# Kernel optimization log

Hardware: AMD Instinct MI355X
Metric: run time of the kernel (lower is better)

The kernel has to match this reference:

```python
import jax, jax.numpy as jnp
import numpy as np

B, C, F, H, W = 8, 16, 256, 112, 112   # batch, cells/image, channels, height, width
NB = 3                                  # tgt_shape = (3, 3) adaptive pool bins


def setup_inputs() -> dict:
    key = jax.random.key(0)
    kf, ky, kx, kry, krx, kn = jax.random.split(key, 6)
    feature_maps = jax.random.normal(kf, (B, F, H, W), jnp.float32)
    N = B * C
    # random rectangular cell blobs with bernoulli interior holes + guaranteed core
    cy = jax.random.randint(ky, (N, 1, 1), 20, H - 20)
    cx = jax.random.randint(kx, (N, 1, 1), 20, W - 20)
    ry = jax.random.randint(kry, (N, 1, 1), 5, 18)
    rx = jax.random.randint(krx, (N, 1, 1), 5, 18)
    yy = jnp.arange(H)[None, :, None]
    xx = jnp.arange(W)[None, None, :]
    rect = (jnp.abs(yy - cy) <= ry) & (jnp.abs(xx - cx) <= rx)
    noise = jax.random.bernoulli(kn, 0.8, (N, H, W))
    core = (jnp.abs(yy - cy) <= 2) & (jnp.abs(xx - cx) <= 2)
    cell_masks = rect & (noise | core)            # [N, H, W] bool, each nonempty
    cell_counts = jnp.full((B,), C, jnp.int32)    # fixed cells per image
    return {"feature_maps": feature_maps, "cell_masks": cell_masks,
            "cell_counts": cell_counts}


def _bin_membership(lo, hi, length):
    # adaptive-pool bin i covers [lo + floor(i*sz/NB), lo + ceil((i+1)*sz/NB))
    i = jnp.arange(NB)
    sz = (hi - lo)[..., None]                      # [B, C, 1]
    start = lo[..., None] + (i * sz) // NB         # [B, C, NB]
    end = lo[..., None] + ((i + 1) * sz + NB - 1) // NB
    pos = jnp.arange(length)
    return (pos >= start[..., None]) & (pos < end[..., None])  # [B, C, NB, L]


def reference(feature_maps, cell_masks, cell_counts):
    Bv, Fv, Hv, Wv = feature_maps.shape
    Cv = cell_masks.shape[0] // Bv
    masks = cell_masks.reshape(Bv, Cv, Hv, Wv)
    # tight bbox per cell (first/last True row and column, exclusive end)
    rows = masks.any(-1)                            # [B, C, H]
    cols = masks.any(-2)                            # [B, C, W]
    y0 = jnp.argmax(rows, -1)
    y1 = Hv - jnp.argmax(rows[..., ::-1], -1)
    x0 = jnp.argmax(cols, -1)
    x1 = Wv - jnp.argmax(cols[..., ::-1], -1)
    ymem = _bin_membership(y0, y1, Hv)              # [B, C, NB, H]
    xmem = _bin_membership(x0, x1, Wv)              # [B, C, NB, W]
    neg = jnp.finfo(feature_maps.dtype).min
    feat = feature_maps[:, None]                    # [B, 1, F, H, W]
    m = masks[:, :, None]                           # [B, C, 1, H, W]
    pooled = []
    for i in range(NB):
        ym = ymem[:, :, i][:, :, None, :, None]     # [B, C, 1, H, 1]
        for j in range(NB):
            xm = xmem[:, :, j][:, :, None, None, :]  # [B, C, 1, 1, W]
            inbin = ym & xm
            # inside bin & mask -> feature; inside bin & ~mask -> 0 (zeroed crop);
            # outside bin -> -inf (excluded from max)
            v = jnp.where(inbin & m, feat, jnp.where(inbin, 0.0, neg))
            pooled.append(v.max((-1, -2)))          # [B, C, F]
    out = jnp.stack(pooled, -1)                     # [B, C, F, 9], index = i*NB + j
    # matches torch pooled.view(-1): flatten order f*9 + i*3 + j
    return out.reshape(Bv * Cv, Fv * NB * NB)
```

## Files before the change

### kernel.cpp

```cpp
#include <hip/hip_runtime.h>
#include <float.h>

#define B_  8
#define C_  16
#define N_  (B_*C_)
#define F_  256
#define H_  112
#define W_  112
#define HW_ (H_*W_)
#define NB_ 3
#define FPW 4
#define WPB 4
#define FPB (FPW*WPB)


__global__ __launch_bounds__(256) void bbox_kernel(const int* __restrict__ mask,
                                                   int* __restrict__ bb) {
    int n = blockIdx.x;
    int t = threadIdx.x;
    __shared__ int rowsAny[H_];
    __shared__ int colsAny[W_];
    __shared__ int smin[256];
    __shared__ int smax[256];
    if (t < H_) rowsAny[t] = 0;
    if (t < W_) colsAny[t] = 0;
    __syncthreads();
    const int* m = mask + (size_t)n * HW_;
    for (int idx = t; idx < HW_; idx += 256) {
        if (m[idx]) {
            int y = idx / W_;
            int x = idx - y * W_;
            rowsAny[y] = 1;
            colsAny[x] = 1;
        }
    }
    __syncthreads();
    smin[t] = (t < H_ && rowsAny[t]) ? t : 0x3fffffff;
    smax[t] = (t < H_ && rowsAny[t]) ? t : -1;
    __syncthreads();
    #pragma unroll
    for (int s = 128; s > 0; s >>= 1) {
        if (t < s) { smin[t] = min(smin[t], smin[t+s]); smax[t] = max(smax[t], smax[t+s]); }
        __syncthreads();
    }
    int y0 = smin[0], y1 = smax[0] + 1;
    __syncthreads();
    smin[t] = (t < W_ && colsAny[t]) ? t : 0x3fffffff;
    smax[t] = (t < W_ && colsAny[t]) ? t : -1;
    __syncthreads();
    #pragma unroll
    for (int s = 128; s > 0; s >>= 1) {
        if (t < s) { smin[t] = min(smin[t], smin[t+s]); smax[t] = max(smax[t], smax[t+s]); }
        __syncthreads();
    }
    if (t == 0) {
        int x0 = smin[0], x1 = smax[0] + 1;
        int* o = bb + n * 16;
        o[0] = y0; o[1] = y1; o[2] = x0; o[3] = x1;
        int szy = y1 - y0, szx = x1 - x0;
        for (int i = 0; i < NB_; ++i) {
            o[4+i]  = y0 + (i*szy)/NB_;
            o[7+i]  = y0 + ((i+1)*szy + NB_-1)/NB_;
            o[10+i] = x0 + (i*szx)/NB_;
            o[13+i] = x0 + ((i+1)*szx + NB_-1)/NB_;
        }
    }
}

__global__ __launch_bounds__(256) void pool_kernel(
        const float* __restrict__ feat, const int* __restrict__ mask,
        const int* __restrict__ bb, float* __restrict__ out) {
    int n = blockIdx.x;
    int b = n >> 4;
    const int* o = bb + n * 16;
    int y0 = o[0], x0 = o[2];
    int bh = o[1] - y0, bw = o[3] - x0;

    __shared__ float lmask[37 * 37];
    {
        const int* mbase = mask + (size_t)n * HW_ + (size_t)y0 * W_ + x0;
        int tot = bh * bw;
        for (int idx = threadIdx.x; idx < tot; idx += 256) {
            int dy = idx / bw, dx = idx - dy * bw;
            lmask[idx] = mbase[dy * W_ + dx] ? 1.0f : 0.0f;
        }
    }
    __syncthreads();

    int wave = threadIdx.x >> 6, lane = threadIdx.x & 63;
    int laneC = lane < bw ? lane : bw - 1;
    int f0 = blockIdx.y * FPB + wave * FPW;
    const float* p = feat + (size_t)(b * F_ + f0) * HW_ + (size_t)y0 * W_ + x0 + laneC;

    int ys0 = o[4], ys1 = o[5], ys2 = o[6];
    int ye0 = o[7], ye1 = o[8], ye2 = o[9];

    float acc[3][FPW];
    #pragma unroll
    for (int i = 0; i < 3; ++i)
        #pragma unroll
        for (int k = 0; k < FPW; ++k) acc[i][k] = -FLT_MAX;

    float fv[FPW];
    #pragma unroll
    for (int k = 0; k < FPW; ++k) fv[k] = p[k * HW_];

    for (int dy = 0; dy < bh; ++dy) {
        int dyn = (dy + 1 < bh) ? dy + 1 : dy;
        int offn = dyn * W_;
        float nv[FPW];
        #pragma unroll
        for (int k = 0; k < FPW; ++k) nv[k] = p[k * HW_ + offn];

        float mv = lmask[dy * bw + laneC];
        int y = y0 + dy;
        bool in0 = (y >= ys0) & (y < ye0);
        bool in1 = (y >= ys1) & (y < ye1);
        bool in2 = (y >= ys2) & (y < ye2);
        #pragma unroll
        for (int k = 0; k < FPW; ++k) {
            float v = mv * fv[k];
            if (in0) acc[0][k] = fmaxf(acc[0][k], v);
            if (in1) acc[1][k] = fmaxf(acc[1][k], v);
            if (in2) acc[2][k] = fmaxf(acc[2][k], v);
        }
        #pragma unroll
        for (int k = 0; k < FPW; ++k) fv[k] = nv[k];
    }

    int x = x0 + lane;
    int xs[3] = {o[10], o[11], o[12]};
    int xe[3] = {o[13], o[14], o[15]};

    #pragma unroll
    for (int k = 0; k < FPW; ++k) {
        float st = 0.0f;
        #pragma unroll
        for (int i = 0; i < 3; ++i) {
            #pragma unroll
            for (int j = 0; j < 3; ++j) {
                float val = (x >= xs[j] && x < xe[j]) ? acc[i][k] : -FLT_MAX;
                #pragma unroll
                for (int off = 32; off; off >>= 1)
                    val = fmaxf(val, __shfl_xor(val, off));
                st = (lane == i * 3 + j) ? val : st;
            }
        }
        if (lane < 9) out[(size_t)(n * F_ + f0 + k) * 9 + lane] = st;
    }
}

extern "C" void kernel_launch(void* const* d_in, const int* in_sizes, int n_in,
                              void* d_out, int out_size, void* d_ws, size_t ws_size,
                              hipStream_t stream) {
    const float* feat = (const float*)d_in[0];
    const int*   mask = (const int*)d_in[1];
    int* bb = (int*)d_ws;

    bbox_kernel<<<N_, 256, 0, stream>>>(mask, bb);
    dim3 grid(N_, F_ / FPB);
    pool_kernel<<<grid, 256, 0, stream>>>(feat, mask, bb, (float*)d_out);
}
```

Measured before the change: 197.4 us.

## Vectorize bbox scan with int4 loads and pool with float4 row tiles

The bbox kernel now reads the mask as int4, keeps per-thread min/max of rows and columns, and reduces them with wave shuffles instead of shared flag arrays and tree reductions. The pool kernel remaps each wave so 16 lanes cover 64 aligned columns with float4 loads and 4 lane groups cover 4 rows per step. It processes 2 channels in parallel over 2 sequential passes, with the shared mask padded to 64 columns. The aim is to cut the number of load instructions and the serial per-row loop, at the cost of more accumulator registers and 9 shuffle reductions per channel.

```diff
diff --git a/kernel.cpp b/kernel.cpp
--- a/kernel.cpp
+++ b/kernel.cpp
@@ -9,52 +9,50 @@
 #define W_  112
 #define HW_ (H_*W_)
 #define NB_ 3
-#define FPW 4
-#define WPB 4
-#define FPB (FPW*WPB)
+
+#define FPAR 2
+#define FSEQ 2
+#define FPW  (FPAR*FSEQ)
+#define WPB  4
+#define FPB  (FPW*WPB)
+#define LMS  64
 
 
-__global__ __launch_bounds__(256) void bbox_kernel(const int* __restrict__ mask,
+__global__ __launch_bounds__(256) void bbox_kernel(const int4* __restrict__ mask4,
                                                    int* __restrict__ bb) {
-    int n = blockIdx.x;
-    int t = threadIdx.x;
-    __shared__ int rowsAny[H_];
-    __shared__ int colsAny[W_];
-    __shared__ int smin[256];
-    __shared__ int smax[256];
-    if (t < H_) rowsAny[t] = 0;
-    if (t < W_) colsAny[t] = 0;
-    __syncthreads();
-    const int* m = mask + (size_t)n * HW_;
-    for (int idx = t; idx < HW_; idx += 256) {
-        if (m[idx]) {
-            int y = idx / W_;
-            int x = idx - y * W_;
-            rowsAny[y] = 1;
-            colsAny[x] = 1;
-        }
+    int n = blockIdx.x, t = threadIdx.x;
+    const int4* m = mask4 + (size_t)n * (HW_ / 4);
+    int ymin = 1 << 20, ymax = -1, xmin = 1 << 20, xmax = -1;
+    for (int i = t; i < HW_ / 4; i += 256) {
+        int4 v = m[i];
+        int y = i / 28;
+        int xb = (i - y * 28) * 4;
+        if (v.x | v.y | v.z | v.w) { ymin = min(ymin, y); ymax = max(ymax, y); }
+        if (v.x) { xmin = min(xmin, xb);     xmax = max(xmax, xb);     }
+        if (v.y) { xmin = min(xmin, xb + 1); xmax = max(xmax, xb + 1); }
+        if (v.z) { xmin = min(xmin, xb + 2); xmax = max(xmax, xb + 2); }
+        if (v.w) { xmin = min(xmin, xb + 3); xmax = max(xmax, xb + 3); }
+    }
+    #pragma unroll
+    for (int off = 32; off; off >>= 1) {
+        ymin = min(ymin, __shfl_xor(ymin, off));
+        ymax = max(ymax, __shfl_xor(ymax, off));
+        xmin = min(xmin, __shfl_xor(xmin, off));
+        xmax = max(xmax, __shfl_xor(xmax, off));
+    }
+    __shared__ int red[4][4];
+    int wave = t >> 6;
+    if ((t & 63) == 0) {
+        red[wave][0] = ymin; red[wave][1] = ymax;
+        red[wave][2] = xmin; red[wave][3] = xmax;
     }
     __syncthreads();
-    smin[t] = (t < H_ && rowsAny[t]) ? t : 0x3fffffff;
-    smax[t] = (t < H_ && rowsAny[t]) ? t : -1;
-    __syncthreads();
-    #pragma unroll
-    for (int s = 128; s > 0; s >>= 1) {
-        if (t < s) { smin[t] = min(smin[t], smin[t+s]); smax[t] = max(smax[t], smax[t+s]); }
-        __syncthreads();
-    }
-    int y0 = smin[0], y1 = smax[0] + 1;
-    __syncthreads();
-    smin[t] = (t < W_ && colsAny[t]) ? t : 0x3fffffff;
-    smax[t] = (t < W_ && colsAny[t]) ? t : -1;
-    __syncthreads();
-    #pragma unroll
-    for (int s = 128; s > 0; s >>= 1) {
-        if (t < s) { smin[t] = min(smin[t], smin[t+s]); smax[t] = max(smax[t], smax[t+s]); }
-        __syncthreads();
-    }
     if (t == 0) {
-        int x0 = smin[0], x1 = smax[0] + 1;
+        for (int w = 1; w < 4; ++w) {
+            ymin = min(ymin, red[w][0]); ymax = max(ymax, red[w][1]);
+            xmin = min(xmin, red[w][2]); xmax = max(xmax, red[w][3]);
+        }
+        int y0 = ymin, y1 = ymax + 1, x0 = xmin, x1 = xmax + 1;
         int* o = bb + n * 16;
         o[0] = y0; o[1] = y1; o[2] = x0; o[3] = x1;
         int szy = y1 - y0, szx = x1 - x0;
@@ -75,78 +73,111 @@
     const int* o = bb + n * 16;
     int y0 = o[0], x0 = o[2];
     int bh = o[1] - y0, bw = o[3] - x0;
+    int x0a = x0 & ~3;
+    int woff = x0 - x0a;
+    int x1 = x0 + bw;
 
-    __shared__ float lmask[37 * 37];
-    {
-        const int* mbase = mask + (size_t)n * HW_ + (size_t)y0 * W_ + x0;
-        int tot = bh * bw;
-        for (int idx = threadIdx.x; idx < tot; idx += 256) {
-            int dy = idx / bw, dx = idx - dy * bw;
-            lmask[idx] = mbase[dy * W_ + dx] ? 1.0f : 0.0f;
-        }
+    __shared__ float lm[37 * LMS];
+    for (int idx = threadIdx.x; idx < bh * LMS; idx += 256) {
+        int dy = idx >> 6, xo = idx & 63;
+        int gx = x0a + xo;
+        float v = 0.0f;
+        if (gx >= x0 && gx < x1)
+            v = mask[(size_t)n * HW_ + (size_t)(y0 + dy) * W_ + gx] ? 1.0f : 0.0f;
+        lm[idx] = v;
     }
     __syncthreads();
 
-    int wave = threadIdx.x >> 6, lane = threadIdx.x & 63;
-    int laneC = lane < bw ? lane : bw - 1;
+    int lane = threadIdx.x & 63, wave = threadIdx.x >> 6;
+    int xq = lane & 15, rg = lane >> 4;
+    int xq4  = (4 * xq < woff + bw) ? 4 * xq : 0;
     int f0 = blockIdx.y * FPB + wave * FPW;
-    const float* p = feat + (size_t)(b * F_ + f0) * HW_ + (size_t)y0 * W_ + x0 + laneC;
 
     int ys0 = o[4], ys1 = o[5], ys2 = o[6];
     int ye0 = o[7], ye1 = o[8], ye2 = o[9];
+    int xs0 = o[10], xs1 = o[11], xs2 = o[12];
+    int xe0 = o[13], xe1 = o[14], xe2 = o[15];
 
-    float acc[3][FPW];
-    #pragma unroll
-    for (int i = 0; i < 3; ++i)
+    int ntiles = (bh + 3) >> 2;
+    int bhm1 = bh - 1;
+    const float* gbase = feat + (size_t)(b * F_) * HW_ + (size_t)y0 * W_ + x0a + xq4;
+
+    for (int fs = 0; fs < FSEQ; ++fs) {
+        int f = f0 + fs * FPAR;
+        const float* gp0 = gbase + (size_t)f * HW_;
+        const float* gp1 = gp0 + HW_;
+
+        float acc[3][4][FPAR];
         #pragma unroll
-        for (int k = 0; k < FPW; ++k) acc[i][k] = -FLT_MAX;
+        for (int i = 0; i < 3; ++i)
+            #pragma unroll
+            for (int s = 0; s < 4; ++s)
+                #pragma unroll
+                for (int pp = 0; pp < FPAR; ++pp) acc[i][s][pp] = -FLT_MAX;
 
-    float fv[FPW];
-    #pragma unroll
-    for (int k = 0; k < FPW; ++k) fv[k] = p[k * HW_];
+        int dy0 = min(rg, bhm1);
+        float4 cur0 = *(const float4*)(gp0 + dy0 * W_);
+        float4 cur1 = *(const float4*)(gp1 + dy0 * W_);
 
-    for (int dy = 0; dy < bh; ++dy) {
-        int dyn = (dy + 1 < bh) ? dy + 1 : dy;
-        int offn = dyn * W_;
-        float nv[FPW];
+        for (int t = 0; t < ntiles; ++t) {
+            int tn = (t + 1 < ntiles) ? t + 1 : t;
+            int dyn = min(4 * tn + rg, bhm1);
+            float4 nxt0 = *(const float4*)(gp0 + dyn * W_);
+            float4 nxt1 = *(const float4*)(gp1 + dyn * W_);
+
+            int dyc = min(4 * t + rg, bhm1);
+            float4 mv = *(const float4*)(&lm[dyc * LMS + 4 * xq]);
+            int y = y0 + dyc;
+            bool in0 = (y >= ys0) & (y < ye0);
+            bool in1 = (y >= ys1) & (y < ye1);
+            bool in2 = (y >= ys2) & (y < ye2);
+
+            float v0[4] = {mv.x * cur0.x, mv.y * cur0.y, mv.z * cur0.z, mv.w * cur0.w};
+            float v1[4] = {mv.x * cur1.x, mv.y * cur1.y, mv.z * cur1.z, mv.w * cur1.w};
+            #pragma unroll
+            for (int s = 0; s < 4; ++s) {
+                if (in0) { acc[0][s][0] = fmaxf(acc[0][s][0], v0[s]);
+                           acc[0][s][1] = fmaxf(acc[0][s][1], v1[s]); }
+                if (in1) { acc[1][s][0] = fmaxf(acc[1][s][0], v0[s]);
+                           acc[1][s][1] = fmaxf(acc[1][s][1], v1[s]); }
+                if (in2) { acc[2][s][0] = fmaxf(acc[2][s][0], v0[s]);
+                           acc[2][s][1] = fmaxf(acc[2][s][1], v1[s]); }
+            }
+            cur0 = nxt0; cur1 = nxt1;
+        }
+
+        int xg = x0a + 4 * xq;
         #pragma unroll
-        for (int k = 0; k < FPW; ++k) nv[k] = p[k * HW_ + offn];
-
-        float mv = lmask[dy * bw + laneC];
-        int y = y0 + dy;
-        bool in0 = (y >= ys0) & (y < ye0);
-        bool in1 = (y >= ys1) & (y < ye1);
-        bool in2 = (y >= ys2) & (y < ye2);
-        #pragma unroll
-        for (int k = 0; k < FPW; ++k) {
-            float v = mv * fv[k];
-            if (in0) acc[0][k] = fmaxf(acc[0][k], v);
-            if (in1) acc[1][k] = fmaxf(acc[1][k], v);
-            if (in2) acc[2][k] = fmaxf(acc[2][k], v);
+        for (int pp = 0; pp < FPAR; ++pp) {
+            float part[9];
+            #pragma unroll
+            for (int i = 0; i < 3; ++i) {
+                #pragma unroll
+                for (int s = 0; s < 4; ++s) {
+                    int xx = xg + s;
+                    float a = acc[i][s][pp];
+                    float p0 = (xx >= xs0 && xx < xe0) ? a : -FLT_MAX;
+                    float p1 = (xx >= xs1 && xx < xe1) ? a : -FLT_MAX;
+                    float p2 = (xx >= xs2 && xx < xe2) ? a : -FLT_MAX;
+                    if (s == 0) { part[i*3+0] = p0; part[i*3+1] = p1; part[i*3+2] = p2; }
+                    else {
+                        part[i*3+0] = fmaxf(part[i*3+0], p0);
+                        part[i*3+1] = fmaxf(part[i*3+1], p1);
+                        part[i*3+2] = fmaxf(part[i*3+2], p2);
+                    }
+                }
+            }
+            #pragma unroll
+            for (int off = 32; off; off >>= 1)
+                #pragma unroll
+                for (int q = 0; q < 9; ++q)
+                    part[q] = fmaxf(part[q], __shfl_xor(part[q], off));
+            float st = part[0];
+            #pragma unroll
+            for (int q = 1; q < 9; ++q) st = (lane == q) ? part[q] : st;
+            if (lane < 9)
+                out[(size_t)(n * F_ + f + pp) * 9 + lane] = st;
         }
-        #pragma unroll
-        for (int k = 0; k < FPW; ++k) fv[k] = nv[k];
-    }
-
-    int x = x0 + lane;
-    int xs[3] = {o[10], o[11], o[12]};
-    int xe[3] = {o[13], o[14], o[15]};
-
-    #pragma unroll
-    for (int k = 0; k < FPW; ++k) {
-        float st = 0.0f;
-        #pragma unroll
-        for (int i = 0; i < 3; ++i) {
-            #pragma unroll
-            for (int j = 0; j < 3; ++j) {
-                float val = (x >= xs[j] && x < xe[j]) ? acc[i][k] : -FLT_MAX;
-                #pragma unroll
-                for (int off = 32; off; off >>= 1)
-                    val = fmaxf(val, __shfl_xor(val, off));
-                st = (lane == i * 3 + j) ? val : st;
-            }
-        }
-        if (lane < 9) out[(size_t)(n * F_ + f0 + k) * 9 + lane] = st;
     }
 }
 
@@ -157,7 +188,7 @@
     const int*   mask = (const int*)d_in[1];
     int* bb = (int*)d_ws;
 
-    bbox_kernel<<<N_, 256, 0, stream>>>(mask, bb);
+    bbox_kernel<<<N_, 256, 0, stream>>>((const int4*)mask, bb);
     dim3 grid(N_, F_ / FPB);
     pool_kernel<<<grid, 256, 0, stream>>>(feat, mask, bb, (float*)d_out);
 }
```

Measured after the change: 184.8 us. -6.4%, faster.
